# Kernel tuning notes

Measured on AMD Instinct MI355X. Metric: run time of the kernel, lower is better.

The kernel has to match this reference:

```python
import jax, jax.numpy as jnp
import numpy as np

BETA = 1.0
EPS = 1e-8  # matches torch F.cosine_similarity eps


def setup_inputs() -> dict:
    key = jax.random.key(0)
    x = jax.random.normal(key, (4096, 2, 1024), dtype=jnp.float32)
    return {"x": x}


def _cosine_sim_matrix(pos, anc):
    # pos: [B, D], anc: [B, D] -> [B, B], sim[i, j] = cos(pos[i], anc[j])
    dots = jnp.einsum('id,jd->ij', pos, anc)
    pn = jnp.sqrt(jnp.sum(pos * pos, axis=-1))
    an = jnp.sqrt(jnp.sum(anc * anc, axis=-1))
    denom = jnp.maximum(pn[:, None] * an[None, :], EPS)
    return dots / denom


def reference(x):
    # x: [B, M, D], M >= 2
    out_anchor = jnp.mean(x[:, 1:, :], axis=1)   # [B, D]
    out_positive = x[:, 0, :]                     # [B, D]
    sim = _cosine_sim_matrix(out_positive, out_anchor)  # [B, B]
    n = sim.shape[0]

    diag = jnp.diagonal(sim)                      # [B]
    # tempsim for column i: beta * (sim[:, i] - sim[i, i]), excluding row i
    T = BETA * (sim - diag[None, :])              # [B, B]
    eye = jnp.eye(n, dtype=bool)

    # exclude-diagonal logsumexp per column (vectorized over all columns)
    Tm = jnp.where(eye, -jnp.inf, T)
    temploss = jax.nn.logsumexp(Tm, axis=0)       # [B]
    # flatNCE trick: exp(l - stop_grad(l)) has value 1 but gradient of l
    nloss = jnp.mean(jnp.exp(temploss - jax.lax.stop_gradient(temploss)))

    # top-1 accuracy against labels arange(B) (detached in original)
    label = jnp.arange(n)
    prec1 = jnp.mean((jnp.argmax(sim, axis=1) == label).astype(jnp.float32)) * 100.0
    return nloss, prec1
```

## Files before the change

kernel.cpp:

```cpp
#include <hip/hip_runtime.h>


#define NROWS 4096
#define DDIM  1024
#define XSTR  2048

typedef unsigned int u32;
typedef unsigned long long u64;
typedef __attribute__((ext_vector_type(8))) short bf16x8;
typedef __attribute__((ext_vector_type(8))) unsigned short u16x8;
typedef __attribute__((ext_vector_type(16))) float f32x16;

__device__ __forceinline__ unsigned int fkey(float f) {
    unsigned int u = __float_as_uint(f);
    return (u & 0x80000000u) ? ~u : (u | 0x80000000u);
}

__device__ __forceinline__ u64 shfl_xor_u64(u64 v, int m) {
    unsigned int lo = (unsigned int)v;
    unsigned int hi = (unsigned int)(v >> 32);
    lo = __shfl_xor(lo, m, 64);
    hi = __shfl_xor(hi, m, 64);
    return ((u64)hi << 32) | lo;
}

__device__ __forceinline__ unsigned short f2bf(float f) {
    unsigned u = __float_as_uint(f);
    return (unsigned short)((u + 0x7FFFu + ((u >> 16) & 1u)) >> 16);
}

#define PF_OFF   0u
#define AF_OFF   8388608u
#define SUM_OFF  16777216u
#define PCK_OFF  16793600u
#define DONE_OFF 16826368u
#define WS_NEED  16826432u
#define ZERO_BYTES (WS_NEED - SUM_OFF)

__global__ __launch_bounds__(256) void conv_kernel(const float* __restrict__ x,
                                                   unsigned short* __restrict__ Pf,
                                                   unsigned short* __restrict__ Af,
                                                   float* __restrict__ sums) {
    __shared__ float rsum[256];
    const int t    = threadIdx.x;
    const int cid  = blockIdx.x * 256 + t;
    const int lane = cid & 63;
    const int kh   = (cid >> 6) & 63;
    const int fb   = cid >> 12;
    const int row  = fb * 32 + (lane & 31);
    const int col  = kh * 16 + (lane >> 5) * 8;

    const float* px = x + (size_t)row * XSTR + col;
    float4 p0 = *(const float4*)(px);
    float4 p1 = *(const float4*)(px + 4);
    float4 a0 = *(const float4*)(px + DDIM);
    float4 a1 = *(const float4*)(px + DDIM + 4);

    u16x8 pv, av;
    pv[0] = f2bf(p0.x); pv[1] = f2bf(p0.y); pv[2] = f2bf(p0.z); pv[3] = f2bf(p0.w);
    pv[4] = f2bf(p1.x); pv[5] = f2bf(p1.y); pv[6] = f2bf(p1.z); pv[7] = f2bf(p1.w);
    av[0] = f2bf(a0.x); av[1] = f2bf(a0.y); av[2] = f2bf(a0.z); av[3] = f2bf(a0.w);
    av[4] = f2bf(a1.x); av[5] = f2bf(a1.y); av[6] = f2bf(a1.z); av[7] = f2bf(a1.w);

    *(u16x8*)(Pf + (size_t)cid * 8) = pv;
    *(u16x8*)(Af + (size_t)cid * 8) = av;

    float s = a0.x * a0.x + a0.y * a0.y + a0.z * a0.z + a0.w * a0.w
            + a1.x * a1.x + a1.y * a1.y + a1.z * a1.z + a1.w * a1.w;
    rsum[t] = s;
    __syncthreads();
    if (t < 32) {
        float tot = 0.0f;
#pragma unroll
        for (int w = 0; w < 8; ++w) tot += rsum[t + 32 * w];
        atomicAdd(&sums[fb * 32 + t], tot);
    }
}

__global__ __launch_bounds__(512, 2) void mfma_gemm_argmax(const unsigned short* __restrict__ Pf,
                                                           const unsigned short* __restrict__ Af,
                                                           const float* __restrict__ sums,
                                                           u64* __restrict__ packed,
                                                           unsigned int* __restrict__ done,
                                                           float* __restrict__ out) {
    __shared__ __align__(16) unsigned int lds[32768];
    __shared__ unsigned int lastflag;
    __shared__ int cnt[8];

    const int bid = blockIdx.x;
    const int xcd = bid & 7;
    const int slt = bid >> 3;
    const int rblk = (xcd >> 1) * 4 + (slt >> 3);
    const int cblk = (xcd & 1) * 8 + (slt & 7);
    const int r0 = rblk * 256;
    const int c0 = cblk * 256;

    const int wave = threadIdx.x >> 6;
    const int lane = threadIdx.x & 63;
    const int l31 = lane & 31;
    const int lh = lane >> 5;
    const int wm = wave & 3;
    const int wn = wave >> 2;

    const char* gPs = (const char*)Pf + (((size_t)(rblk * 8 + wave)) << 16) + (size_t)lane * 16;
    const char* gAs = (const char*)Af + (((size_t)(cblk * 8 + wave)) << 16) + (size_t)lane * 16;

    f32x16 zero16 = {0.f,0.f,0.f,0.f,0.f,0.f,0.f,0.f,0.f,0.f,0.f,0.f,0.f,0.f,0.f,0.f};
    f32x16 acc[2][4];
#pragma unroll
    for (int i = 0; i < 2; ++i)
#pragma unroll
        for (int j = 0; j < 4; ++j) acc[i][j] = zero16;

#pragma unroll
    for (int kh_l = 0; kh_l < 4; ++kh_l) {
        __builtin_amdgcn_global_load_lds((const u32*)(gPs + ((size_t)kh_l << 10)),
                                         &lds[kh_l * 2048 + wave * 256], 16, 0, 0);
        __builtin_amdgcn_global_load_lds((const u32*)(gAs + ((size_t)kh_l << 10)),
                                         &lds[8192 + kh_l * 2048 + wave * 256], 16, 0, 0);
    }

    for (int t = 0; t < 16; ++t) {
        const int cb = t & 1;
        const int nbuf = (cb ^ 1) * 16384;
        const int cbuf = cb * 16384;

        asm volatile("s_waitcnt vmcnt(0)" ::: "memory");
        __builtin_amdgcn_s_barrier();
        __builtin_amdgcn_sched_barrier(0);

#pragma unroll
        for (int kh_l = 0; kh_l < 4; ++kh_l) {
            const u32* bp = &lds[cbuf + kh_l * 2048 + (wm * 2) * 256 + lane * 4];
            bf16x8 f_p0 = *(const bf16x8*)(bp);
            bf16x8 f_p1 = *(const bf16x8*)(bp + 256);
            const u32* ba = &lds[cbuf + 8192 + kh_l * 2048 + (wn * 4) * 256 + lane * 4];
            bf16x8 f_a0 = *(const bf16x8*)(ba);
            bf16x8 f_a1 = *(const bf16x8*)(ba + 256);
            bf16x8 f_a2 = *(const bf16x8*)(ba + 512);
            bf16x8 f_a3 = *(const bf16x8*)(ba + 768);

            if (t + 1 < 16) {
                const size_t go = ((size_t)((t + 1) * 4 + kh_l)) << 10;
                __builtin_amdgcn_global_load_lds((const u32*)(gPs + go),
                                                 &lds[nbuf + kh_l * 2048 + wave * 256], 16, 0, 0);
                __builtin_amdgcn_global_load_lds((const u32*)(gAs + go),
                                                 &lds[nbuf + 8192 + kh_l * 2048 + wave * 256], 16, 0, 0);
            }

            __builtin_amdgcn_s_barrier();
            asm volatile("s_waitcnt lgkmcnt(0)" ::: "memory");
            __builtin_amdgcn_sched_barrier(0);
            __builtin_amdgcn_s_setprio(1);
            acc[0][0] = __builtin_amdgcn_mfma_f32_32x32x16_bf16(f_p0, f_a0, acc[0][0], 0, 0, 0);
            acc[0][1] = __builtin_amdgcn_mfma_f32_32x32x16_bf16(f_p0, f_a1, acc[0][1], 0, 0, 0);
            acc[0][2] = __builtin_amdgcn_mfma_f32_32x32x16_bf16(f_p0, f_a2, acc[0][2], 0, 0, 0);
            acc[0][3] = __builtin_amdgcn_mfma_f32_32x32x16_bf16(f_p0, f_a3, acc[0][3], 0, 0, 0);
            acc[1][0] = __builtin_amdgcn_mfma_f32_32x32x16_bf16(f_p1, f_a0, acc[1][0], 0, 0, 0);
            acc[1][1] = __builtin_amdgcn_mfma_f32_32x32x16_bf16(f_p1, f_a1, acc[1][1], 0, 0, 0);
            acc[1][2] = __builtin_amdgcn_mfma_f32_32x32x16_bf16(f_p1, f_a2, acc[1][2], 0, 0, 0);
            acc[1][3] = __builtin_amdgcn_mfma_f32_32x32x16_bf16(f_p1, f_a3, acc[1][3], 0, 0, 0);
            __builtin_amdgcn_s_setprio(0);
            __builtin_amdgcn_s_barrier();
        }
    }

    float ian[4];
#pragma unroll
    for (int nt = 0; nt < 4; ++nt) ian[nt] = 1.0f / sqrtf(sums[c0 + wn * 128 + nt * 32 + l31]);

#pragma unroll
    for (int mt = 0; mt < 2; ++mt)
#pragma unroll
        for (int reg = 0; reg < 16; ++reg) {
            const int row = r0 + wm * 64 + mt * 32 + (reg & 3) + 8 * (reg >> 2) + 4 * lh;
            u64 best = 0ULL;
#pragma unroll
            for (int nt = 0; nt < 4; ++nt) {
                const int col = c0 + wn * 128 + nt * 32 + l31;
                const float v = acc[mt][nt][reg] * ian[nt];
                const u64 p = ((u64)fkey(v) << 32) | (unsigned int)(~col);
                best = best > p ? best : p;
            }
#pragma unroll
            for (int m = 1; m <= 16; m <<= 1) {
                const u64 o = shfl_xor_u64(best, m);
                best = best > o ? best : o;
            }
            if (l31 == 0) atomicMax(&packed[row], best);
        }

    __syncthreads();
    if (threadIdx.x == 0) {
        __threadfence();
        unsigned int old = atomicAdd(done, 1u);
        lastflag = (old == 255u) ? 1u : 0u;
    }
    __syncthreads();
    if (lastflag) {
        int c = 0;
        for (int r = threadIdx.x; r < NROWS; r += 512) {
            u64 v = atomicAdd(&packed[r], 0ULL);
            unsigned int col = ~(unsigned int)(v & 0xFFFFFFFFULL);
            c += (col == (unsigned int)r) ? 1 : 0;
        }
#pragma unroll
        for (int off = 32; off > 0; off >>= 1) c += __shfl_down(c, off, 64);
        if ((threadIdx.x & 63) == 0) cnt[threadIdx.x >> 6] = c;
        __syncthreads();
        if (threadIdx.x == 0) {
            int tot = 0;
#pragma unroll
            for (int w = 0; w < 8; ++w) tot += cnt[w];
            out[0] = 1.0f;
            out[1] = 100.0f * (float)tot / (float)NROWS;
        }
    }
}

__global__ __launch_bounds__(256) void norms_kernel(const float* __restrict__ x,
                                                    float* __restrict__ inv_an,
                                                    u64* __restrict__ packed) {
    int gid  = blockIdx.x * 256 + threadIdx.x;
    int j    = gid >> 6;
    int lane = threadIdx.x & 63;
    if (gid < NROWS) packed[gid] = 0ULL;
    const float4* a = (const float4*)(x + (size_t)j * XSTR + DDIM);
    float s = 0.0f;
#pragma unroll
    for (int i = 0; i < 4; ++i) {
        float4 v = a[lane + i * 64];
        s += v.x * v.x + v.y * v.y + v.z * v.z + v.w * v.w;
    }
#pragma unroll
    for (int off = 32; off > 0; off >>= 1) s += __shfl_down(s, off, 64);
    if (lane == 0) inv_an[j] = 1.0f / sqrtf(s);
}

__global__ __launch_bounds__(256) void gemm_argmax_kernel(const float* __restrict__ x,
                                                          const float* __restrict__ inv_an,
                                                          u64* __restrict__ packed) {
    __shared__ __align__(16) float Pt[16][128];
    __shared__ __align__(16) float At[16][128];
    const int r0 = blockIdx.x * 128;
    const int c0 = blockIdx.y * 128;
    const int t = threadIdx.x;
    const int tx = t & 15;
    const int ty = t >> 4;
    const int srow = t >> 1;
    const int skq = (t & 1) * 8;
    float acc[8][8];
#pragma unroll
    for (int r = 0; r < 8; ++r)
#pragma unroll
        for (int c = 0; c < 8; ++c) acc[r][c] = 0.0f;
    const float* gp = x + (size_t)(r0 + srow) * XSTR + skq;
    const float* ga = x + (size_t)(c0 + srow) * XSTR + DDIM + skq;
    for (int k0 = 0; k0 < DDIM; k0 += 16) {
        __syncthreads();
        float4 p0 = *(const float4*)(gp + k0);
        float4 p1 = *(const float4*)(gp + k0 + 4);
        float4 a0 = *(const float4*)(ga + k0);
        float4 a1 = *(const float4*)(ga + k0 + 4);
        Pt[skq + 0][srow] = p0.x; Pt[skq + 1][srow] = p0.y;
        Pt[skq + 2][srow] = p0.z; Pt[skq + 3][srow] = p0.w;
        Pt[skq + 4][srow] = p1.x; Pt[skq + 5][srow] = p1.y;
        Pt[skq + 6][srow] = p1.z; Pt[skq + 7][srow] = p1.w;
        At[skq + 0][srow] = a0.x; At[skq + 1][srow] = a0.y;
        At[skq + 2][srow] = a0.z; At[skq + 3][srow] = a0.w;
        At[skq + 4][srow] = a1.x; At[skq + 5][srow] = a1.y;
        At[skq + 6][srow] = a1.z; At[skq + 7][srow] = a1.w;
        __syncthreads();
#pragma unroll
        for (int kk = 0; kk < 16; ++kk) {
            float pr[8], ar[8];
            *(float4*)&pr[0] = *(const float4*)&Pt[kk][ty * 8];
            *(float4*)&pr[4] = *(const float4*)&Pt[kk][ty * 8 + 4];
            *(float4*)&ar[0] = *(const float4*)&At[kk][tx * 8];
            *(float4*)&ar[4] = *(const float4*)&At[kk][tx * 8 + 4];
#pragma unroll
            for (int r = 0; r < 8; ++r)
#pragma unroll
                for (int c = 0; c < 8; ++c) acc[r][c] += pr[r] * ar[c];
        }
    }
    float ian[8];
#pragma unroll
    for (int c = 0; c < 8; ++c) ian[c] = inv_an[c0 + tx * 8 + c];
#pragma unroll
    for (int r = 0; r < 8; ++r) {
        int row = r0 + ty * 8 + r;
        u64 best = 0ULL;
#pragma unroll
        for (int c = 0; c < 8; ++c) {
            int col = c0 + tx * 8 + c;
            float v = acc[r][c] * ian[c];
            u64 p = ((u64)fkey(v) << 32) | (unsigned int)(~col);
            best = best > p ? best : p;
        }
#pragma unroll
        for (int m = 1; m <= 8; m <<= 1) {
            u64 o = shfl_xor_u64(best, m);
            best = best > o ? best : o;
        }
        if (tx == 0) atomicMax(&packed[row], best);
    }
}

__global__ __launch_bounds__(256) void finalize_kernel(const u64* __restrict__ packed,
                                                       float* __restrict__ out) {
    __shared__ int cnt_s;
    int t = threadIdx.x;
    if (t == 0) cnt_s = 0;
    __syncthreads();
    int c = 0;
    for (int r = t; r < NROWS; r += 256) {
        unsigned int col = ~(unsigned int)(packed[r] & 0xFFFFFFFFULL);
        c += (col == (unsigned int)r) ? 1 : 0;
    }
#pragma unroll
    for (int off = 32; off > 0; off >>= 1) c += __shfl_down(c, off, 64);
    if ((t & 63) == 0) atomicAdd(&cnt_s, c);
    __syncthreads();
    if (t == 0) {
        out[0] = 1.0f;
        out[1] = 100.0f * (float)cnt_s / (float)NROWS;
    }
}

extern "C" void kernel_launch(void* const* d_in, const int* in_sizes, int n_in,
                              void* d_out, int out_size, void* d_ws, size_t ws_size,
                              hipStream_t stream) {
    (void)in_sizes; (void)n_in; (void)out_size;
    const float* x = (const float*)d_in[0];
    float* out = (float*)d_out;

    if (ws_size >= (size_t)WS_NEED) {
        char* ws = (char*)d_ws;
        unsigned short* Pf = (unsigned short*)(ws + PF_OFF);
        unsigned short* Af = (unsigned short*)(ws + AF_OFF);
        float* sums = (float*)(ws + SUM_OFF);
        u64* packed = (u64*)(ws + PCK_OFF);
        unsigned int* done = (unsigned int*)(ws + DONE_OFF);

        hipMemsetAsync(ws + SUM_OFF, 0, (size_t)ZERO_BYTES, stream);
        conv_kernel<<<2048, 256, 0, stream>>>(x, Pf, Af, sums);
        mfma_gemm_argmax<<<256, 512, 0, stream>>>(Pf, Af, sums, packed, done, out);
    } else {
        float* inv_an = (float*)d_ws;
        u64* packed = (u64*)((char*)d_ws + NROWS * sizeof(float));
        norms_kernel<<<NROWS / 4, 256, 0, stream>>>(x, inv_an, packed);
        dim3 grid(NROWS / 128, NROWS / 128);
        gemm_argmax_kernel<<<grid, 256, 0, stream>>>(x, inv_an, packed);
        finalize_kernel<<<1, 256, 0, stream>>>(packed, out);
    }
}
```

Before: 121.5 us.

## Fuse fp32-to-bf16 conversion and anchor norms into the GEMM-argmax kernel

Removes the separate conversion kernel and its bf16 workspace round trip. The GEMM now reads fp32 rows of x directly into registers, converts them to bf16 and stores them to LDS after the MFMAs of each k-step, so the next tile's loads overlap with compute. Anchor squared norms are accumulated in registers and reduced through LDS instead of with global atomics. The costs are reading twice as many bytes per tile (fp32 instead of bf16), extra VGPRs held across the MFMAs, and conversion ALU work inside the main loop; the workspace memset is now much smaller.

```diff
diff --git a/kernel.cpp b/kernel.cpp
--- a/kernel.cpp
+++ b/kernel.cpp
@@ -29,61 +29,16 @@
     return (unsigned short)((u + 0x7FFFu + ((u >> 16) & 1u)) >> 16);
 }
 
-#define PF_OFF   0u
-#define AF_OFF   8388608u
-#define SUM_OFF  16777216u
-#define PCK_OFF  16793600u
-#define DONE_OFF 16826368u
-#define WS_NEED  16826432u
-#define ZERO_BYTES (WS_NEED - SUM_OFF)
-
-__global__ __launch_bounds__(256) void conv_kernel(const float* __restrict__ x,
-                                                   unsigned short* __restrict__ Pf,
-                                                   unsigned short* __restrict__ Af,
-                                                   float* __restrict__ sums) {
-    __shared__ float rsum[256];
-    const int t    = threadIdx.x;
-    const int cid  = blockIdx.x * 256 + t;
-    const int lane = cid & 63;
-    const int kh   = (cid >> 6) & 63;
-    const int fb   = cid >> 12;
-    const int row  = fb * 32 + (lane & 31);
-    const int col  = kh * 16 + (lane >> 5) * 8;
-
-    const float* px = x + (size_t)row * XSTR + col;
-    float4 p0 = *(const float4*)(px);
-    float4 p1 = *(const float4*)(px + 4);
-    float4 a0 = *(const float4*)(px + DDIM);
-    float4 a1 = *(const float4*)(px + DDIM + 4);
-
-    u16x8 pv, av;
-    pv[0] = f2bf(p0.x); pv[1] = f2bf(p0.y); pv[2] = f2bf(p0.z); pv[3] = f2bf(p0.w);
-    pv[4] = f2bf(p1.x); pv[5] = f2bf(p1.y); pv[6] = f2bf(p1.z); pv[7] = f2bf(p1.w);
-    av[0] = f2bf(a0.x); av[1] = f2bf(a0.y); av[2] = f2bf(a0.z); av[3] = f2bf(a0.w);
-    av[4] = f2bf(a1.x); av[5] = f2bf(a1.y); av[6] = f2bf(a1.z); av[7] = f2bf(a1.w);
-
-    *(u16x8*)(Pf + (size_t)cid * 8) = pv;
-    *(u16x8*)(Af + (size_t)cid * 8) = av;
-
-    float s = a0.x * a0.x + a0.y * a0.y + a0.z * a0.z + a0.w * a0.w
-            + a1.x * a1.x + a1.y * a1.y + a1.z * a1.z + a1.w * a1.w;
-    rsum[t] = s;
-    __syncthreads();
-    if (t < 32) {
-        float tot = 0.0f;
-#pragma unroll
-        for (int w = 0; w < 8; ++w) tot += rsum[t + 32 * w];
-        atomicAdd(&sums[fb * 32 + t], tot);
-    }
-}
-
-__global__ __launch_bounds__(512, 2) void mfma_gemm_argmax(const unsigned short* __restrict__ Pf,
-                                                           const unsigned short* __restrict__ Af,
-                                                           const float* __restrict__ sums,
+#define PCK_OFF  0u
+#define DONE_OFF 32768u
+#define WS_NEED  32832u
+
+__global__ __launch_bounds__(512, 2) void mfma_gemm_argmax(const float* __restrict__ x,
                                                            u64* __restrict__ packed,
                                                            unsigned int* __restrict__ done,
                                                            float* __restrict__ out) {
     __shared__ __align__(16) unsigned int lds[32768];
+    __shared__ float sums_s[256];
     __shared__ unsigned int lastflag;
     __shared__ int cnt[8];
 
@@ -102,8 +57,10 @@
     const int wm = wave & 3;
     const int wn = wave >> 2;
 
-    const char* gPs = (const char*)Pf + (((size_t)(rblk * 8 + wave)) << 16) + (size_t)lane * 16;
-    const char* gAs = (const char*)Af + (((size_t)(cblk * 8 + wave)) << 16) + (size_t)lane * 16;
+    const int prow = (rblk * 8 + wave) * 32 + l31;
+    const int arow = (cblk * 8 + wave) * 32 + l31;
+    const float* gPx = x + (size_t)prow * XSTR + lh * 8;
+    const float* gAx = x + (size_t)arow * XSTR + DDIM + lh * 8;
 
     f32x16 zero16 = {0.f,0.f,0.f,0.f,0.f,0.f,0.f,0.f,0.f,0.f,0.f,0.f,0.f,0.f,0.f,0.f};
     f32x16 acc[2][4];
@@ -112,12 +69,34 @@
 #pragma unroll
         for (int j = 0; j < 4; ++j) acc[i][j] = zero16;
 
+    float sq = 0.0f;
+
+#define LOADCH(kh, pv0, pv1, av0, av1)                                                  \
+    {                                                                                   \
+        const float* pp_ = gPx + (kh) * 16;                                             \
+        const float* aa_ = gAx + (kh) * 16;                                             \
+        pv0 = *(const float4*)(pp_);  pv1 = *(const float4*)(pp_ + 4);                  \
+        av0 = *(const float4*)(aa_);  av1 = *(const float4*)(aa_ + 4);                  \
+    }
+
+#define WRITECH(bb, kh_l, pv0, pv1, av0, av1)                                           \
+    {                                                                                   \
+        u16x8 pc_, ac_;                                                                 \
+        pc_[0] = f2bf(pv0.x); pc_[1] = f2bf(pv0.y); pc_[2] = f2bf(pv0.z); pc_[3] = f2bf(pv0.w); \
+        pc_[4] = f2bf(pv1.x); pc_[5] = f2bf(pv1.y); pc_[6] = f2bf(pv1.z); pc_[7] = f2bf(pv1.w); \
+        ac_[0] = f2bf(av0.x); ac_[1] = f2bf(av0.y); ac_[2] = f2bf(av0.z); ac_[3] = f2bf(av0.w); \
+        ac_[4] = f2bf(av1.x); ac_[5] = f2bf(av1.y); ac_[6] = f2bf(av1.z); ac_[7] = f2bf(av1.w); \
+        *(u16x8*)&lds[(bb) + (kh_l) * 2048 + wave * 256 + lane * 4] = pc_;              \
+        *(u16x8*)&lds[(bb) + 8192 + (kh_l) * 2048 + wave * 256 + lane * 4] = ac_;       \
+        sq += av0.x * av0.x + av0.y * av0.y + av0.z * av0.z + av0.w * av0.w             \
+            + av1.x * av1.x + av1.y * av1.y + av1.z * av1.z + av1.w * av1.w;            \
+    }
+
 #pragma unroll
     for (int kh_l = 0; kh_l < 4; ++kh_l) {
-        __builtin_amdgcn_global_load_lds((const u32*)(gPs + ((size_t)kh_l << 10)),
-                                         &lds[kh_l * 2048 + wave * 256], 16, 0, 0);
-        __builtin_amdgcn_global_load_lds((const u32*)(gAs + ((size_t)kh_l << 10)),
-                                         &lds[8192 + kh_l * 2048 + wave * 256], 16, 0, 0);
+        float4 pv0, pv1, av0, av1;
+        LOADCH(kh_l, pv0, pv1, av0, av1)
+        WRITECH(0, kh_l, pv0, pv1, av0, av1)
     }
 
     for (int t = 0; t < 16; ++t) {
@@ -125,12 +104,15 @@
         const int nbuf = (cb ^ 1) * 16384;
         const int cbuf = cb * 16384;
 
-        asm volatile("s_waitcnt vmcnt(0)" ::: "memory");
+        asm volatile("s_waitcnt lgkmcnt(0)" ::: "memory");
         __builtin_amdgcn_s_barrier();
         __builtin_amdgcn_sched_barrier(0);
 
 #pragma unroll
         for (int kh_l = 0; kh_l < 4; ++kh_l) {
+            float4 pv0, pv1, av0, av1;
+            if (t + 1 < 16) LOADCH((t + 1) * 4 + kh_l, pv0, pv1, av0, av1)
+
             const u32* bp = &lds[cbuf + kh_l * 2048 + (wm * 2) * 256 + lane * 4];
             bf16x8 f_p0 = *(const bf16x8*)(bp);
             bf16x8 f_p1 = *(const bf16x8*)(bp + 256);
@@ -139,14 +121,6 @@
             bf16x8 f_a1 = *(const bf16x8*)(ba + 256);
             bf16x8 f_a2 = *(const bf16x8*)(ba + 512);
             bf16x8 f_a3 = *(const bf16x8*)(ba + 768);
-
-            if (t + 1 < 16) {
-                const size_t go = ((size_t)((t + 1) * 4 + kh_l)) << 10;
-                __builtin_amdgcn_global_load_lds((const u32*)(gPs + go),
-                                                 &lds[nbuf + kh_l * 2048 + wave * 256], 16, 0, 0);
-                __builtin_amdgcn_global_load_lds((const u32*)(gAs + go),
-                                                 &lds[nbuf + 8192 + kh_l * 2048 + wave * 256], 16, 0, 0);
-            }
 
             __builtin_amdgcn_s_barrier();
             asm volatile("s_waitcnt lgkmcnt(0)" ::: "memory");
@@ -161,13 +135,24 @@
             acc[1][2] = __builtin_amdgcn_mfma_f32_32x32x16_bf16(f_p1, f_a2, acc[1][2], 0, 0, 0);
             acc[1][3] = __builtin_amdgcn_mfma_f32_32x32x16_bf16(f_p1, f_a3, acc[1][3], 0, 0, 0);
             __builtin_amdgcn_s_setprio(0);
+
+            if (t + 1 < 16) WRITECH(nbuf, kh_l, pv0, pv1, av0, av1)
+
             __builtin_amdgcn_s_barrier();
         }
     }
+#undef LOADCH
+#undef WRITECH
+
+    {
+        float st = sq + __shfl_xor(sq, 32, 64);
+        if (lane < 32) sums_s[wave * 32 + lane] = st;
+    }
+    __syncthreads();
 
     float ian[4];
 #pragma unroll
-    for (int nt = 0; nt < 4; ++nt) ian[nt] = 1.0f / sqrtf(sums[c0 + wn * 128 + nt * 32 + l31]);
+    for (int nt = 0; nt < 4; ++nt) ian[nt] = 1.0f / sqrtf(sums_s[wn * 128 + nt * 32 + l31]);
 
 #pragma unroll
     for (int mt = 0; mt < 2; ++mt)
@@ -337,15 +322,11 @@
 
     if (ws_size >= (size_t)WS_NEED) {
         char* ws = (char*)d_ws;
-        unsigned short* Pf = (unsigned short*)(ws + PF_OFF);
-        unsigned short* Af = (unsigned short*)(ws + AF_OFF);
-        float* sums = (float*)(ws + SUM_OFF);
         u64* packed = (u64*)(ws + PCK_OFF);
         unsigned int* done = (unsigned int*)(ws + DONE_OFF);
 
-        hipMemsetAsync(ws + SUM_OFF, 0, (size_t)ZERO_BYTES, stream);
-        conv_kernel<<<2048, 256, 0, stream>>>(x, Pf, Af, sums);
-        mfma_gemm_argmax<<<256, 512, 0, stream>>>(Pf, Af, sums, packed, done, out);
+        hipMemsetAsync(ws, 0, (size_t)WS_NEED, stream);
+        mfma_gemm_argmax<<<256, 512, 0, stream>>>(x, packed, done, out);
     } else {
         float* inv_an = (float*)d_ws;
         u64* packed = (u64*)((char*)d_ws + NROWS * sizeof(float));
```

After: 162.5 us. 1.34x slower.
